# Performance work log

Measured on AMD Instinct MI355X. Metric: run time of the kernel, lower is better.

## Reference

```python
import jax, jax.numpy as jnp
import numpy as np

EPS = 1e-5

def setup_inputs() -> dict:
    key = jax.random.key(0)
    ks = jax.random.split(key, 10)
    B, S, C, Q, D = 16, 2048, 768, 1024, 64
    clamp3_features = jax.random.normal(ks[0], (B, S, C), dtype=jnp.float32)
    residual = jax.random.normal(ks[1], (B, S, Q), dtype=jnp.float32)
    # params (xavier-ish scale; up-proj given small random values instead of zeros
    # so the output is non-trivial for correctness testing)
    Wproj = jax.random.normal(ks[2], (Q, C), dtype=jnp.float32) * (1.0 / np.sqrt(C))
    Wdown = jax.random.normal(ks[3], (D, Q), dtype=jnp.float32) * (1.0 / np.sqrt(Q))
    gamma = jnp.ones((D,), dtype=jnp.float32)
    beta = jnp.zeros((D,), dtype=jnp.float32)
    Wl1 = jax.random.normal(ks[4], (D, D), dtype=jnp.float32) * (1.0 / np.sqrt(D))
    bl1 = jnp.zeros((D,), dtype=jnp.float32)
    Wl2 = jax.random.normal(ks[5], (D, D), dtype=jnp.float32) * (1.0 / np.sqrt(D))
    bl2 = jnp.zeros((D,), dtype=jnp.float32)
    Wup = jax.random.normal(ks[6], (Q, D), dtype=jnp.float32) * (1.0 / np.sqrt(D))
    return {"clamp3_features": clamp3_features, "residual": residual,
            "Wproj": Wproj, "Wdown": Wdown, "gamma": gamma, "beta": beta,
            "Wl1": Wl1, "bl1": bl1, "Wl2": Wl2, "bl2": bl2, "Wup": Wup}

def _layernorm(x, gamma, beta):
    mu = jnp.mean(x, axis=-1, keepdims=True)
    var = jnp.mean(jnp.square(x - mu), axis=-1, keepdims=True)
    return (x - mu) * jax.lax.rsqrt(var + EPS) * gamma + beta

def reference(clamp3_features, residual, Wproj, Wdown, gamma, beta, Wl1, bl1, Wl2, bl2, Wup):
    # projection (no bias) -> down (no bias) -> LayerNorm
    projected = jnp.einsum('bsc,qc->bsq', clamp3_features, Wproj)
    down = jnp.einsum('bsq,dq->bsd', projected, Wdown)
    normed = _layernorm(down, gamma, beta)
    # SwiGLU: swish(l1(x)) * l2(x)
    o1 = jnp.einsum('bsd,ed->bse', normed, Wl1) + bl1
    swish = o1 * jax.nn.sigmoid(o1)
    gate = jnp.einsum('bsd,ed->bse', normed, Wl2) + bl2
    activated = swish * gate  # dropout is identity in eval mode
    up = jnp.einsum('bsd,qd->bsq', activated, Wup)
    return residual + up
```

## Files before the change

### kernel.cpp

```cpp
#include <hip/hip_runtime.h>


#define CDIM 768
#define QDIM 1024

typedef __attribute__((ext_vector_type(8))) short bf16x8;
typedef __attribute__((ext_vector_type(4))) float f32x4;

__device__ __forceinline__ ushort f2bf(float f) {
  union { float f; unsigned u; } v; v.f = f;
  unsigned r = v.u + 0x7fffu + ((v.u >> 16) & 1u);
  return (ushort)(r >> 16);
}

__global__ void k_wcomb(const float* __restrict__ Wproj, const float* __restrict__ Wdown,
                        float* __restrict__ part) {
  int bid = blockIdx.x;
  int cb = bid % 12, db = (bid / 12) % 8, qc = bid / 96;
  int l = threadIdx.x;
  int c = cb * 64 + l;
  float acc[8];
  #pragma unroll
  for (int i = 0; i < 8; ++i) acc[i] = 0.f;
  int q0 = qc * 128;
  for (int q = q0; q < q0 + 128; ++q) {
    float xp = Wproj[q * CDIM + c];
    #pragma unroll
    for (int i = 0; i < 8; ++i)
      acc[i] = fmaf(Wdown[(db * 8 + i) * QDIM + q], xp, acc[i]);
  }
  #pragma unroll
  for (int i = 0; i < 8; ++i)
    part[((size_t)qc * CDIM + c) * 64 + db * 8 + i] = acc[i];
}

__global__ void k_arrange(const float* __restrict__ part, const float* __restrict__ Wup,
                          const float* __restrict__ Wl1, const float* __restrict__ Wl2,
                          ushort* __restrict__ wcf, ushort* __restrict__ wupf,
                          ushort* __restrict__ wl1f, ushort* __restrict__ wl2f) {
  int idx = blockIdx.x * 256 + threadIdx.x;
  if (idx < 49152) {
    int i0 = idx;
    int j = i0 & 7, l = (i0 >> 3) & 63, t = i0 >> 9;
    int g = l >> 4, r16 = l & 15;
    int nf = t & 3, ks = t >> 2;
    int k = 32 * ks + 8 * g + j, n = 16 * nf + r16;
    float s = 0.f;
    #pragma unroll
    for (int qc = 0; qc < 8; ++qc) s += part[((size_t)qc * CDIM + k) * 64 + n];
    wcf[i0] = f2bf(s);
  } else if (idx < 49152 + 65536) {
    int i2 = idx - 49152;
    int j = i2 & 7, l = (i2 >> 3) & 63, t = i2 >> 9;
    int g = l >> 4, r16 = l & 15;
    int ks = t & 1, nf = t >> 1;
    int k = 32 * ks + 8 * g + j, n = 16 * nf + r16;
    wupf[i2] = f2bf(Wup[n * 64 + k]);
  } else if (idx < 49152 + 65536 + 4096) {
    int i3 = idx - (49152 + 65536);
    int j = i3 & 7, l = (i3 >> 3) & 63, t = i3 >> 9;
    int g = l >> 4, r16 = l & 15;
    int nf = t & 3, ks = t >> 2;
    int k = 32 * ks + 8 * g + j, e = 16 * nf + r16;
    wl1f[i3] = f2bf(Wl1[e * 64 + k]);
  } else {
    int i4 = idx - (49152 + 65536 + 4096);
    int j = i4 & 7, l = (i4 >> 3) & 63, t = i4 >> 9;
    int g = l >> 4, r16 = l & 15;
    int nf = t & 3, ks = t >> 2;
    int k = 32 * ks + 8 * g + j, e = 16 * nf + r16;
    wl2f[i4] = f2bf(Wl2[e * 64 + k]);
  }
}

__global__ __launch_bounds__(256, 6)
void k_act(const float* __restrict__ xg,
           const float* __restrict__ gamma, const float* __restrict__ beta,
           const float* __restrict__ bl1, const float* __restrict__ bl2,
           const ushort* __restrict__ wcf,
           const ushort* __restrict__ wl1f, const ushort* __restrict__ wl2f,
           ushort* __restrict__ ag) {
  __shared__ ushort smem[12416];
  ushort (*x_lds)[776] = reinterpret_cast<ushort(*)[776]>(smem);
  float  (*d_lds)[68]  = reinterpret_cast<float (*)[68]>(smem);
  ushort (*n_lds)[72]  = reinterpret_cast<ushort(*)[72]>(reinterpret_cast<char*>(smem) + 4608);

  const int tid = threadIdx.x;
  const int w = tid >> 6, l = tid & 63, g = l >> 4, r16 = l & 15;
  const int row0 = blockIdx.x * 16;

  #pragma unroll
  for (int i = 0; i < 12; ++i) {
    int f4 = i * 256 + tid;
    int r = f4 / 192;
    int c4 = (f4 - r * 192) * 4;
    const float4 v = *reinterpret_cast<const float4*>(xg + (size_t)(row0 + r) * CDIM + c4);
    ushort4 b;
    b.x = f2bf(v.x); b.y = f2bf(v.y); b.z = f2bf(v.z); b.w = f2bf(v.w);
    *reinterpret_cast<ushort4*>(&x_lds[r][c4]) = b;
  }
  __syncthreads();

  f32x4 dacc = {0.f, 0.f, 0.f, 0.f};
  #pragma unroll 8
  for (int ks = 0; ks < 24; ++ks) {
    bf16x8 a = *reinterpret_cast<const bf16x8*>(&x_lds[r16][ks * 32 + 8 * g]);
    bf16x8 b = *reinterpret_cast<const bf16x8*>(wcf + ((size_t)(ks * 4 + w) * 64 + l) * 8);
    dacc = __builtin_amdgcn_mfma_f32_16x16x32_bf16(a, b, dacc, 0, 0, 0);
  }
  __syncthreads();
  #pragma unroll
  for (int rg = 0; rg < 4; ++rg) d_lds[4 * g + rg][16 * w + r16] = dacc[rg];
  __syncthreads();

  {
    int row = 4 * w + g;
    f32x4 v = *reinterpret_cast<const f32x4*>(&d_lds[row][4 * r16]);
    float s  = v[0] + v[1] + v[2] + v[3];
    float sq = v[0]*v[0] + v[1]*v[1] + v[2]*v[2] + v[3]*v[3];
    #pragma unroll
    for (int m = 1; m < 16; m <<= 1) {
      s  += __shfl_xor(s, m, 64);
      sq += __shfl_xor(sq, m, 64);
    }
    float mu  = s * (1.f / 64.f);
    float var = sq * (1.f / 64.f) - mu * mu;
    float rs  = rsqrtf(var + 1e-5f);
    const float4 gm = *reinterpret_cast<const float4*>(gamma + 4 * r16);
    const float4 bt = *reinterpret_cast<const float4*>(beta  + 4 * r16);
    ushort4 nb;
    nb.x = f2bf((v[0] - mu) * rs * gm.x + bt.x);
    nb.y = f2bf((v[1] - mu) * rs * gm.y + bt.y);
    nb.z = f2bf((v[2] - mu) * rs * gm.z + bt.z);
    nb.w = f2bf((v[3] - mu) * rs * gm.w + bt.w);
    *reinterpret_cast<ushort4*>(&n_lds[row][4 * r16]) = nb;
  }
  __syncthreads();

  {
    bf16x8 a0 = *reinterpret_cast<const bf16x8*>(&n_lds[r16][8 * g]);
    bf16x8 a1 = *reinterpret_cast<const bf16x8*>(&n_lds[r16][32 + 8 * g]);
    bf16x8 b10 = *reinterpret_cast<const bf16x8*>(wl1f + ((size_t)(0 * 4 + w) * 64 + l) * 8);
    bf16x8 b11 = *reinterpret_cast<const bf16x8*>(wl1f + ((size_t)(1 * 4 + w) * 64 + l) * 8);
    bf16x8 b20 = *reinterpret_cast<const bf16x8*>(wl2f + ((size_t)(0 * 4 + w) * 64 + l) * 8);
    bf16x8 b21 = *reinterpret_cast<const bf16x8*>(wl2f + ((size_t)(1 * 4 + w) * 64 + l) * 8);
    f32x4 z = {0.f, 0.f, 0.f, 0.f};
    f32x4 acc1 = __builtin_amdgcn_mfma_f32_16x16x32_bf16(a0, b10, z, 0, 0, 0);
    acc1 = __builtin_amdgcn_mfma_f32_16x16x32_bf16(a1, b11, acc1, 0, 0, 0);
    f32x4 acc2 = __builtin_amdgcn_mfma_f32_16x16x32_bf16(a0, b20, z, 0, 0, 0);
    acc2 = __builtin_amdgcn_mfma_f32_16x16x32_bf16(a1, b21, acc2, 0, 0, 0);
    float bv1 = bl1[16 * w + r16];
    float bv2 = bl2[16 * w + r16];
    #pragma unroll
    for (int rg = 0; rg < 4; ++rg) {
      float o1 = acc1[rg] + bv1;
      float o2 = acc2[rg] + bv2;
      float sw = o1 / (1.f + __expf(-o1));
      ag[(size_t)(row0 + 4 * g + rg) * 64 + 16 * w + r16] = f2bf(sw * o2);
    }
  }
}

__global__ __launch_bounds__(256, 3)
void k_up(const ushort* __restrict__ ag, const float* __restrict__ resg,
          const ushort* __restrict__ wupf, float* __restrict__ outg) {
  __shared__ ushort a_lds[16][68];
  const int tid = threadIdx.x;
  const int w = tid >> 6, l = tid & 63, g = l >> 4, r16 = l & 15;
  const int row0 = blockIdx.x * 16;

  {
    int e = tid * 4;
    int r = e >> 6, c = e & 63;
    ushort4 v = *reinterpret_cast<const ushort4*>(ag + (size_t)(row0 + r) * 64 + c);
    *reinterpret_cast<ushort4*>(&a_lds[r][c]) = v;
  }

  const float* rbase = resg + (size_t)(row0 + r16) * QDIM + 256 * w + 4 * g;
  float*       obase = outg + (size_t)(row0 + r16) * QDIM + 256 * w + 4 * g;

  float4 rv[16];
  #pragma unroll
  for (int nfl = 0; nfl < 16; ++nfl)
    rv[nfl] = *reinterpret_cast<const float4*>(rbase + 16 * nfl);
  __builtin_amdgcn_sched_barrier(0);

  __syncthreads();
  const bf16x8 af0 = *reinterpret_cast<const bf16x8*>(&a_lds[r16][8 * g]);
  const bf16x8 af1 = *reinterpret_cast<const bf16x8*>(&a_lds[r16][32 + 8 * g]);

  #pragma unroll
  for (int nfl = 0; nfl < 16; ++nfl) {
    size_t nf = 16 * w + nfl;
    bf16x8 b0 = *reinterpret_cast<const bf16x8*>(wupf + ((nf * 2 + 0) * 64 + l) * 8);
    bf16x8 b1 = *reinterpret_cast<const bf16x8*>(wupf + ((nf * 2 + 1) * 64 + l) * 8);
    f32x4 t = {0.f, 0.f, 0.f, 0.f};
    t = __builtin_amdgcn_mfma_f32_16x16x32_bf16(b0, af0, t, 0, 0, 0);
    t = __builtin_amdgcn_mfma_f32_16x16x32_bf16(b1, af1, t, 0, 0, 0);
    float4 o;
    o.x = rv[nfl].x + t[0]; o.y = rv[nfl].y + t[1];
    o.z = rv[nfl].z + t[2]; o.w = rv[nfl].w + t[3];
    *reinterpret_cast<float4*>(obase + 16 * nfl) = o;
  }
}

extern "C" void kernel_launch(void* const* d_in, const int* in_sizes, int n_in,
                              void* d_out, int out_size, void* d_ws, size_t ws_size,
                              hipStream_t stream) {
  (void)in_sizes; (void)n_in; (void)out_size; (void)ws_size;
  const float* x     = (const float*)d_in[0];
  const float* resid = (const float*)d_in[1];
  const float* Wproj = (const float*)d_in[2];
  const float* Wdown = (const float*)d_in[3];
  const float* gamma = (const float*)d_in[4];
  const float* beta  = (const float*)d_in[5];
  const float* Wl1   = (const float*)d_in[6];
  const float* bl1   = (const float*)d_in[7];
  const float* Wl2   = (const float*)d_in[8];
  const float* bl2   = (const float*)d_in[9];
  const float* Wup   = (const float*)d_in[10];
  float* out = (float*)d_out;

  char* ws = (char*)d_ws;
  float*  part = (float*)(ws);
  ushort* wcf  = (ushort*)(ws + 1572864);
  ushort* wupf = (ushort*)(ws + 1671168);
  ushort* wl1f = (ushort*)(ws + 1802240);
  ushort* wl2f = (ushort*)(ws + 1810432);
  ushort* ag   = (ushort*)(ws + 1818624);

  k_wcomb  <<<768, 64, 0, stream>>>(Wproj, Wdown, part);
  k_arrange<<<480, 256, 0, stream>>>(part, Wup, Wl1, Wl2, wcf, wupf, wl1f, wl2f);
  k_act    <<<2048, 256, 0, stream>>>(x, gamma, beta, bl1, bl2, wcf, wl1f, wl2f, ag);
  k_up     <<<2048, 256, 0, stream>>>(ag, resid, wupf, out);
}
```

Baseline: 127.3 us.

## Fuse activation and up-projection kernels into one, keeping intermediate in LDS

```diff
diff --git a/kernel.cpp b/kernel.cpp
--- a/kernel.cpp
+++ b/kernel.cpp
@@ -73,36 +73,55 @@
   }
 }
 
-__global__ __launch_bounds__(256, 6)
-void k_act(const float* __restrict__ xg,
-           const float* __restrict__ gamma, const float* __restrict__ beta,
-           const float* __restrict__ bl1, const float* __restrict__ bl2,
-           const ushort* __restrict__ wcf,
-           const ushort* __restrict__ wl1f, const ushort* __restrict__ wl2f,
-           ushort* __restrict__ ag) {
+__global__ __launch_bounds__(256, 3)
+void k_main(const float* __restrict__ xg, const float* __restrict__ resg,
+            const float* __restrict__ gamma, const float* __restrict__ beta,
+            const float* __restrict__ bl1, const float* __restrict__ bl2,
+            const ushort* __restrict__ wcf, const ushort* __restrict__ wupf,
+            const ushort* __restrict__ wl1f, const ushort* __restrict__ wl2f,
+            float* __restrict__ outg) {
   __shared__ ushort smem[12416];
   ushort (*x_lds)[776] = reinterpret_cast<ushort(*)[776]>(smem);
   float  (*d_lds)[68]  = reinterpret_cast<float (*)[68]>(smem);
   ushort (*n_lds)[72]  = reinterpret_cast<ushort(*)[72]>(reinterpret_cast<char*>(smem) + 4608);
+  ushort (*a_lds)[72]  = reinterpret_cast<ushort(*)[72]>(reinterpret_cast<char*>(smem) + 8192);
 
   const int tid = threadIdx.x;
   const int w = tid >> 6, l = tid & 63, g = l >> 4, r16 = l & 15;
   const int row0 = blockIdx.x * 16;
 
+  float4 xv[12];
   #pragma unroll
   for (int i = 0; i < 12; ++i) {
     int f4 = i * 256 + tid;
     int r = f4 / 192;
     int c4 = (f4 - r * 192) * 4;
-    const float4 v = *reinterpret_cast<const float4*>(xg + (size_t)(row0 + r) * CDIM + c4);
+    xv[i] = *reinterpret_cast<const float4*>(xg + (size_t)(row0 + r) * CDIM + c4);
+  }
+  #pragma unroll
+  for (int i = 0; i < 12; ++i) {
+    int f4 = i * 256 + tid;
+    int r = f4 / 192;
+    int c4 = (f4 - r * 192) * 4;
     ushort4 b;
-    b.x = f2bf(v.x); b.y = f2bf(v.y); b.z = f2bf(v.z); b.w = f2bf(v.w);
+    b.x = f2bf(xv[i].x); b.y = f2bf(xv[i].y); b.z = f2bf(xv[i].z); b.w = f2bf(xv[i].w);
     *reinterpret_cast<ushort4*>(&x_lds[r][c4]) = b;
   }
+
+  const float* rbase = resg + (size_t)(row0 + r16) * QDIM + 256 * w + 4 * g;
+  f32x4 rv[16];
+  #pragma unroll
+  for (int nfl = 0; nfl < 16; ++nfl)
+    rv[nfl] = *reinterpret_cast<const f32x4*>(rbase + 16 * nfl);
+  #pragma unroll
+  for (int nfl = 0; nfl < 16; ++nfl)
+    asm volatile("" : "+v"(rv[nfl]));
+  __builtin_amdgcn_sched_barrier(0);
+
   __syncthreads();
 
   f32x4 dacc = {0.f, 0.f, 0.f, 0.f};
-  #pragma unroll 8
+  #pragma unroll 4
   for (int ks = 0; ks < 24; ++ks) {
     bf16x8 a = *reinterpret_cast<const bf16x8*>(&x_lds[r16][ks * 32 + 8 * g]);
     bf16x8 b = *reinterpret_cast<const bf16x8*>(wcf + ((size_t)(ks * 4 + w) * 64 + l) * 8);
@@ -156,51 +175,26 @@
       float o1 = acc1[rg] + bv1;
       float o2 = acc2[rg] + bv2;
       float sw = o1 / (1.f + __expf(-o1));
-      ag[(size_t)(row0 + 4 * g + rg) * 64 + 16 * w + r16] = f2bf(sw * o2);
+      a_lds[4 * g + rg][16 * w + r16] = f2bf(sw * o2);
     }
   }
-}
-
-__global__ __launch_bounds__(256, 3)
-void k_up(const ushort* __restrict__ ag, const float* __restrict__ resg,
-          const ushort* __restrict__ wupf, float* __restrict__ outg) {
-  __shared__ ushort a_lds[16][68];
-  const int tid = threadIdx.x;
-  const int w = tid >> 6, l = tid & 63, g = l >> 4, r16 = l & 15;
-  const int row0 = blockIdx.x * 16;
+  __syncthreads();
 
   {
-    int e = tid * 4;
-    int r = e >> 6, c = e & 63;
-    ushort4 v = *reinterpret_cast<const ushort4*>(ag + (size_t)(row0 + r) * 64 + c);
-    *reinterpret_cast<ushort4*>(&a_lds[r][c]) = v;
-  }
-
-  const float* rbase = resg + (size_t)(row0 + r16) * QDIM + 256 * w + 4 * g;
-  float*       obase = outg + (size_t)(row0 + r16) * QDIM + 256 * w + 4 * g;
-
-  float4 rv[16];
-  #pragma unroll
-  for (int nfl = 0; nfl < 16; ++nfl)
-    rv[nfl] = *reinterpret_cast<const float4*>(rbase + 16 * nfl);
-  __builtin_amdgcn_sched_barrier(0);
-
-  __syncthreads();
-  const bf16x8 af0 = *reinterpret_cast<const bf16x8*>(&a_lds[r16][8 * g]);
-  const bf16x8 af1 = *reinterpret_cast<const bf16x8*>(&a_lds[r16][32 + 8 * g]);
-
-  #pragma unroll
-  for (int nfl = 0; nfl < 16; ++nfl) {
-    size_t nf = 16 * w + nfl;
-    bf16x8 b0 = *reinterpret_cast<const bf16x8*>(wupf + ((nf * 2 + 0) * 64 + l) * 8);
-    bf16x8 b1 = *reinterpret_cast<const bf16x8*>(wupf + ((nf * 2 + 1) * 64 + l) * 8);
-    f32x4 t = {0.f, 0.f, 0.f, 0.f};
-    t = __builtin_amdgcn_mfma_f32_16x16x32_bf16(b0, af0, t, 0, 0, 0);
-    t = __builtin_amdgcn_mfma_f32_16x16x32_bf16(b1, af1, t, 0, 0, 0);
-    float4 o;
-    o.x = rv[nfl].x + t[0]; o.y = rv[nfl].y + t[1];
-    o.z = rv[nfl].z + t[2]; o.w = rv[nfl].w + t[3];
-    *reinterpret_cast<float4*>(obase + 16 * nfl) = o;
+    const bf16x8 af0 = *reinterpret_cast<const bf16x8*>(&a_lds[r16][8 * g]);
+    const bf16x8 af1 = *reinterpret_cast<const bf16x8*>(&a_lds[r16][32 + 8 * g]);
+    float* obase = outg + (size_t)(row0 + r16) * QDIM + 256 * w + 4 * g;
+    #pragma unroll
+    for (int nfl = 0; nfl < 16; ++nfl) {
+      size_t nf = 16 * w + nfl;
+      bf16x8 b0 = *reinterpret_cast<const bf16x8*>(wupf + ((nf * 2 + 0) * 64 + l) * 8);
+      bf16x8 b1 = *reinterpret_cast<const bf16x8*>(wupf + ((nf * 2 + 1) * 64 + l) * 8);
+      f32x4 t = {0.f, 0.f, 0.f, 0.f};
+      t = __builtin_amdgcn_mfma_f32_16x16x32_bf16(b0, af0, t, 0, 0, 0);
+      t = __builtin_amdgcn_mfma_f32_16x16x32_bf16(b1, af1, t, 0, 0, 0);
+      f32x4 o = rv[nfl] + t;
+      *reinterpret_cast<f32x4*>(obase + 16 * nfl) = o;
+    }
   }
 }
 
@@ -227,10 +221,9 @@
   ushort* wupf = (ushort*)(ws + 1671168);
   ushort* wl1f = (ushort*)(ws + 1802240);
   ushort* wl2f = (ushort*)(ws + 1810432);
-  ushort* ag   = (ushort*)(ws + 1818624);
 
   k_wcomb  <<<768, 64, 0, stream>>>(Wproj, Wdown, part);
   k_arrange<<<480, 256, 0, stream>>>(part, Wup, Wl1, Wl2, wcf, wupf, wl1f, wl2f);
-  k_act    <<<2048, 256, 0, stream>>>(x, gamma, beta, bl1, bl2, wcf, wl1f, wl2f, ag);
-  k_up     <<<2048, 256, 0, stream>>>(ag, resid, wupf, out);
-}
+  k_main   <<<2048, 256, 0, stream>>>(x, resid, gamma, beta, bl1, bl2,
+                                      wcf, wupf, wl1f, wl2f, out);
+}
```

New measurement: 121.0 us. 1.05x faster.

## Stage activation and up-projection outputs through LDS for coalesced global access

Applied to the files above, without the earlier changes.

```diff
diff --git a/kernel.cpp b/kernel.cpp
--- a/kernel.cpp
+++ b/kernel.cpp
@@ -84,6 +84,7 @@
   ushort (*x_lds)[776] = reinterpret_cast<ushort(*)[776]>(smem);
   float  (*d_lds)[68]  = reinterpret_cast<float (*)[68]>(smem);
   ushort (*n_lds)[72]  = reinterpret_cast<ushort(*)[72]>(reinterpret_cast<char*>(smem) + 4608);
+  ushort (*a_lds)[72]  = reinterpret_cast<ushort(*)[72]>(reinterpret_cast<char*>(smem) + 8192);
 
   const int tid = threadIdx.x;
   const int w = tid >> 6, l = tid & 63, g = l >> 4, r16 = l & 15;
@@ -156,14 +157,22 @@
       float o1 = acc1[rg] + bv1;
       float o2 = acc2[rg] + bv2;
       float sw = o1 / (1.f + __expf(-o1));
-      ag[(size_t)(row0 + 4 * g + rg) * 64 + 16 * w + r16] = f2bf(sw * o2);
-    }
+      a_lds[4 * g + rg][16 * w + r16] = f2bf(sw * o2);
+    }
+  }
+  __syncthreads();
+
+  if (tid < 128) {
+    int r = tid >> 3, c = 8 * (tid & 7);
+    bf16x8 v = *reinterpret_cast<const bf16x8*>(&a_lds[r][c]);
+    *reinterpret_cast<bf16x8*>(ag + (size_t)(row0 + r) * 64 + c) = v;
   }
 }
 
 __global__ __launch_bounds__(256, 3)
 void k_up(const ushort* __restrict__ ag, const float* __restrict__ resg,
           const ushort* __restrict__ wupf, float* __restrict__ outg) {
+  __shared__ float  bounce[16][512];
   __shared__ ushort a_lds[16][68];
   const int tid = threadIdx.x;
   const int w = tid >> 6, l = tid & 63, g = l >> 4, r16 = l & 15;
@@ -175,32 +184,38 @@
     ushort4 v = *reinterpret_cast<const ushort4*>(ag + (size_t)(row0 + r) * 64 + c);
     *reinterpret_cast<ushort4*>(&a_lds[r][c]) = v;
   }
-
-  const float* rbase = resg + (size_t)(row0 + r16) * QDIM + 256 * w + 4 * g;
-  float*       obase = outg + (size_t)(row0 + r16) * QDIM + 256 * w + 4 * g;
-
-  float4 rv[16];
-  #pragma unroll
-  for (int nfl = 0; nfl < 16; ++nfl)
-    rv[nfl] = *reinterpret_cast<const float4*>(rbase + 16 * nfl);
-  __builtin_amdgcn_sched_barrier(0);
-
   __syncthreads();
   const bf16x8 af0 = *reinterpret_cast<const bf16x8*>(&a_lds[r16][8 * g]);
   const bf16x8 af1 = *reinterpret_cast<const bf16x8*>(&a_lds[r16][32 + 8 * g]);
 
   #pragma unroll
-  for (int nfl = 0; nfl < 16; ++nfl) {
-    size_t nf = 16 * w + nfl;
-    bf16x8 b0 = *reinterpret_cast<const bf16x8*>(wupf + ((nf * 2 + 0) * 64 + l) * 8);
-    bf16x8 b1 = *reinterpret_cast<const bf16x8*>(wupf + ((nf * 2 + 1) * 64 + l) * 8);
-    f32x4 t = {0.f, 0.f, 0.f, 0.f};
-    t = __builtin_amdgcn_mfma_f32_16x16x32_bf16(b0, af0, t, 0, 0, 0);
-    t = __builtin_amdgcn_mfma_f32_16x16x32_bf16(b1, af1, t, 0, 0, 0);
-    float4 o;
-    o.x = rv[nfl].x + t[0]; o.y = rv[nfl].y + t[1];
-    o.z = rv[nfl].z + t[2]; o.w = rv[nfl].w + t[3];
-    *reinterpret_cast<float4*>(obase + 16 * nfl) = o;
+  for (int p = 0; p < 2; ++p) {
+    f32x4 acc[8];
+    #pragma unroll
+    for (int i = 0; i < 8; ++i) {
+      size_t nf = 32 * p + 8 * w + i;
+      bf16x8 b0 = *reinterpret_cast<const bf16x8*>(wupf + ((nf * 2 + 0) * 64 + l) * 8);
+      bf16x8 b1 = *reinterpret_cast<const bf16x8*>(wupf + ((nf * 2 + 1) * 64 + l) * 8);
+      f32x4 t = {0.f, 0.f, 0.f, 0.f};
+      t = __builtin_amdgcn_mfma_f32_16x16x32_bf16(b0, af0, t, 0, 0, 0);
+      acc[i] = __builtin_amdgcn_mfma_f32_16x16x32_bf16(b1, af1, t, 0, 0, 0);
+    }
+    if (p) __syncthreads();
+    #pragma unroll
+    for (int i = 0; i < 8; ++i) {
+      int q = 32 * w + 4 * i + g;
+      *reinterpret_cast<f32x4*>(&bounce[r16][4 * (q ^ (r16 & 7))]) = acc[i];
+    }
+    __syncthreads();
+    #pragma unroll
+    for (int s = 0; s < 8; ++s) {
+      int row = 2 * s + (tid >> 7);
+      int cq  = tid & 127;
+      size_t goff = (size_t)(row0 + row) * QDIM + 512 * p + 4 * cq;
+      f32x4 rv = *reinterpret_cast<const f32x4*>(resg + goff);
+      f32x4 bv = *reinterpret_cast<const f32x4*>(&bounce[row][4 * (cq ^ (row & 7))]);
+      *reinterpret_cast<f32x4*>(outg + goff) = rv + bv;
+    }
   }
 }
 
```

Measured after the change: 126.1 us. Within noise of the previous version (-0.9%).
